# Kernel optimization log

Measured on AMD Instinct MI355X. Metric: run time of the kernel, lower is better.

## Reference

```python
import jax, jax.numpy as jnp
import numpy as np

D, NH, NL, NP, NLAYERS, DFF = 256, 8, 4, 4, 6, 1024
HD = D // NH
SHAPES = [(100, 100), (50, 50), (25, 25), (13, 13)]  # (H, W) per level
B = 4


def layernorm(x, w, b):
    m = x.mean(-1, keepdims=True)
    v = ((x - m) ** 2).mean(-1, keepdims=True)
    return (x - m) / jnp.sqrt(v + 1e-5) * w + b


def bilinear_sample(vl, loc, H, W):
    # vl: [B, H*W, NH, HD] level values; loc: [B, Lq, NH, NP, 2] normalized in [0,1]
    # matches F.grid_sample(bilinear, zeros padding, align_corners=False)
    bsz, Lq = loc.shape[0], loc.shape[1]
    px = loc[..., 0] * W - 0.5
    py = loc[..., 1] * H - 0.5
    x0 = jnp.floor(px); y0 = jnp.floor(py)
    wx1 = px - x0; wy1 = py - y0
    out = jnp.zeros((bsz, Lq, NH, NP, HD), vl.dtype)
    for xi, wx in ((x0, 1.0 - wx1), (x0 + 1.0, wx1)):
        for yi, wy in ((y0, 1.0 - wy1), (y0 + 1.0, wy1)):
            valid = (xi >= 0) & (xi < W) & (yi >= 0) & (yi < H)
            xc = jnp.clip(xi, 0, W - 1).astype(jnp.int32)
            yc = jnp.clip(yi, 0, H - 1).astype(jnp.int32)
            idx = yc * W + xc                                   # [B,Lq,NH,NP]
            idx2 = idx.transpose(0, 1, 3, 2).reshape(bsz, Lq * NP, NH, 1)
            g = jnp.take_along_axis(vl, idx2, axis=1)           # [B,Lq*NP,NH,HD]
            g = g.reshape(bsz, Lq, NP, NH, HD).transpose(0, 1, 3, 2, 4)
            w = (wx * wy * valid.astype(vl.dtype))[..., None]
            out = out + g * w
    return out


def get_reference_points(bsz):
    refs = []
    for (H, W) in SHAPES:
        ry = (jnp.arange(H, dtype=jnp.float32) + 0.5) / H
        rx = (jnp.arange(W, dtype=jnp.float32) + 0.5) / W
        gy, gx = jnp.meshgrid(ry, rx, indexing='ij')
        refs.append(jnp.stack([gx.reshape(-1), gy.reshape(-1)], -1))
    ref = jnp.concatenate(refs, 0)                              # [Len, 2]
    return jnp.broadcast_to(ref[None, :, None, :], (bsz, ref.shape[0], NL, 2))


def ms_deform_attn(query, src, ref, starts, so_w, so_b, aw_w, aw_b, vp_w, vp_b, op_w, op_b):
    bsz, Lq, _ = query.shape
    value = (src @ vp_w + vp_b).reshape(bsz, -1, NH, HD)
    offsets = (query @ so_w + so_b).reshape(bsz, Lq, NH, NL, NP, 2)
    aw = (query @ aw_w + aw_b).reshape(bsz, Lq, NH, NL * NP)
    aw = jax.nn.softmax(aw, -1).reshape(bsz, Lq, NH, NL, NP)
    normalizer = jnp.array([[W, H] for (H, W) in SHAPES], jnp.float32)  # x by W, y by H
    loc = ref[:, :, None, :, None, :] + offsets / normalizer[None, None, None, :, None, :]
    out = jnp.zeros((bsz, Lq, NH, HD), query.dtype)
    for l, (H, W) in enumerate(SHAPES):
        vl = value[:, starts[l]:starts[l] + H * W]
        sampled = bilinear_sample(vl, loc[:, :, :, l], H, W)    # [B,Lq,NH,NP,HD]
        out = out + jnp.einsum('blhp,blhpd->blhd', aw[:, :, :, l], sampled)
    return out.reshape(bsz, Lq, D) @ op_w + op_b


def setup_inputs():
    key = jax.random.key(0)
    ks = iter(jax.random.split(key, 64))
    d = {}
    for i, (H, W) in enumerate(SHAPES):
        d[f'src{i}'] = jax.random.normal(next(ks), (B, D, H, W), jnp.float32)
        d[f'pos{i}'] = jax.random.normal(next(ks), (B, D, H, W), jnp.float32)
    d['level_embed'] = jax.random.normal(next(ks), (NL, D), jnp.float32)
    d['so_w'] = jax.random.normal(next(ks), (NLAYERS, D, NH * NL * NP * 2), jnp.float32) * 0.005
    d['so_b'] = jax.random.normal(next(ks), (NLAYERS, NH * NL * NP * 2), jnp.float32) * 0.1
    d['aw_w'] = jax.random.normal(next(ks), (NLAYERS, D, NH * NL * NP), jnp.float32) * 0.02
    d['aw_b'] = jnp.zeros((NLAYERS, NH * NL * NP), jnp.float32)
    d['vp_w'] = jax.random.normal(next(ks), (NLAYERS, D, D), jnp.float32) * 0.02
    d['vp_b'] = jnp.zeros((NLAYERS, D), jnp.float32)
    d['op_w'] = jax.random.normal(next(ks), (NLAYERS, D, D), jnp.float32) * 0.02
    d['op_b'] = jnp.zeros((NLAYERS, D), jnp.float32)
    d['n1_w'] = jnp.ones((NLAYERS, D), jnp.float32)
    d['n1_b'] = jnp.zeros((NLAYERS, D), jnp.float32)
    d['f1_w'] = jax.random.normal(next(ks), (NLAYERS, D, DFF), jnp.float32) * 0.02
    d['f1_b'] = jnp.zeros((NLAYERS, DFF), jnp.float32)
    d['f2_w'] = jax.random.normal(next(ks), (NLAYERS, DFF, D), jnp.float32) * 0.02
    d['f2_b'] = jnp.zeros((NLAYERS, D), jnp.float32)
    d['n2_w'] = jnp.ones((NLAYERS, D), jnp.float32)
    d['n2_b'] = jnp.zeros((NLAYERS, D), jnp.float32)
    return d


def reference(src0, src1, src2, src3, pos0, pos1, pos2, pos3, level_embed,
              so_w, so_b, aw_w, aw_b, vp_w, vp_b, op_w, op_b,
              n1_w, n1_b, f1_w, f1_b, f2_w, f2_b, n2_w, n2_b):
    srcs = [src0, src1, src2, src3]
    poss = [pos0, pos1, pos2, pos3]
    bsz = src0.shape[0]
    src_flat, pos_flat, starts, off = [], [], [], 0
    for l, ((H, W), s, p) in enumerate(zip(SHAPES, srcs, poss)):
        starts.append(off); off += H * W
        src_flat.append(s.reshape(bsz, D, H * W).transpose(0, 2, 1))
        pos_flat.append(p.reshape(bsz, D, H * W).transpose(0, 2, 1) + level_embed[l][None, None, :])
    src = jnp.concatenate(src_flat, 1)                          # [B, Len, D]
    pos = jnp.concatenate(pos_flat, 1)
    ref = get_reference_points(bsz)
    for i in range(NLAYERS):
        q = src + pos
        attn = ms_deform_attn(q, src, ref, starts,
                              so_w[i], so_b[i], aw_w[i], aw_b[i],
                              vp_w[i], vp_b[i], op_w[i], op_b[i])
        src = layernorm(src + attn, n1_w[i], n1_b[i])
        h = jax.nn.relu(src @ f1_w[i] + f1_b[i]) @ f2_w[i] + f2_b[i]
        src = layernorm(src + h, n2_w[i], n2_b[i])
    level_start_index = jnp.array(starts, jnp.int64 if jax.config.jax_enable_x64 else jnp.int32)
    return src, level_start_index
```

## Files before the change

### kernel.cpp

```cpp
#include <hip/hip_runtime.h>

#define D 256
#define L_TOT 13294

typedef __attribute__((ext_vector_type(8))) __bf16 bf16x8;
typedef __attribute__((ext_vector_type(4))) float f32x4;
typedef __attribute__((ext_vector_type(2))) float f32x2;

__device__ __forceinline__ float bf2f(unsigned short u) {
    return __uint_as_float(((unsigned int)u) << 16);
}
__device__ __forceinline__ unsigned short f2bf(float f) {
    unsigned int u = __float_as_uint(f);
    u += 0x7FFFu + ((u >> 16) & 1u);
    return (unsigned short)(u >> 16);
}
__device__ __forceinline__ f32x2 bfpair(unsigned int d) {
    f32x2 r;
    r.x = __uint_as_float(d << 16);
    r.y = __uint_as_float(d & 0xFFFF0000u);
    return r;
}
__device__ __forceinline__ f32x2 fma2(f32x2 a, float w, f32x2 c) {
    return __builtin_elementwise_fma(a, (f32x2){w, w}, c);
}

__global__ void probe_k(const unsigned short* __restrict__ u, int n, int* __restrict__ flag)
{
    __shared__ int cnt;
    if (threadIdx.x == 0) cnt = 0;
    __syncthreads();
    int c = 0;
    for (int i = threadIdx.x; i < n; i += 256) {
        const int e = (u[i] >> 7) & 0xFF;
        if (e == 0 || (e >= 96 && e <= 150)) ++c;
    }
    atomicAdd(&cnt, c);
    __syncthreads();
    if (threadIdx.x == 0) *flag = (cnt * 10 > n * 9) ? 1 : 0;
}

__global__ __launch_bounds__(256) void convert_k(
    const void* __restrict__ src, unsigned short* __restrict__ dst, int n,
    const int* __restrict__ flag)
{
    const int i = blockIdx.x * 256 + threadIdx.x;
    if (i >= n) return;
    if (*flag) dst[i] = ((const unsigned short*)src)[i];
    else       dst[i] = f2bf(((const float*)src)[i]);
}

__global__ __launch_bounds__(256) void convt_k(
    const void* __restrict__ src, unsigned short* __restrict__ dst,
    int K, int N, int L, const int* __restrict__ flag)
{
    const long e = (long)blockIdx.x * 256 + threadIdx.x;
    const long tot = (long)L * K * N;
    if (e >= tot) return;
    const int per = K * N;
    const int li = (int)(e / per);
    const int r  = (int)(e - (long)li * per);
    const int n  = r / K;
    const int k  = r - n * K;
    const long s = (long)li * per + (long)k * N + n;
    dst[e] = (*flag) ? ((const unsigned short*)src)[s]
                     : f2bf(((const float*)src)[s]);
}

__global__ __launch_bounds__(256) void flatten_k(
    const void* __restrict__ s0, const void* __restrict__ s1,
    const void* __restrict__ s2, const void* __restrict__ s3,
    const int* __restrict__ flag, unsigned short* __restrict__ state)
{
    const long e = (long)blockIdx.x * 256 + threadIdx.x;
    const int d = (int)(e & 255);
    const long tok = e >> 8;
    const int b = (int)(tok / L_TOT);
    const int t = (int)(tok - (long)b * L_TOT);
    const void *sp;
    int hw, idx;
    if (t < 10000)      { sp = s0; hw = 10000; idx = t;          }
    else if (t < 12500) { sp = s1; hw = 2500;  idx = t - 10000;  }
    else if (t < 13125) { sp = s2; hw = 625;   idx = t - 12500;  }
    else                { sp = s3; hw = 169;   idx = t - 13125;  }
    const long a = ((long)b * D + d) * hw + idx;
    state[e] = (*flag) ? ((const unsigned short*)sp)[a]
                       : f2bf(((const float*)sp)[a]);
}

__global__ __launch_bounds__(256) void posconst_k(
    const void* __restrict__ p0, const void* __restrict__ p1,
    const void* __restrict__ p2, const void* __restrict__ p3,
    const unsigned short* __restrict__ lev, const int* __restrict__ flag,
    unsigned short* __restrict__ posc)
{
    const long e = (long)blockIdx.x * 256 + threadIdx.x;
    const int d = (int)(e & 255);
    const long tok = e >> 8;
    const int b = (int)(tok / L_TOT);
    const int t = (int)(tok - (long)b * L_TOT);
    const void *pp;
    int hw, idx, l;
    if (t < 10000)      { pp = p0; hw = 10000; idx = t;          l = 0; }
    else if (t < 12500) { pp = p1; hw = 2500;  idx = t - 10000;  l = 1; }
    else if (t < 13125) { pp = p2; hw = 625;   idx = t - 12500;  l = 2; }
    else                { pp = p3; hw = 169;   idx = t - 13125;  l = 3; }
    const long a = ((long)b * D + d) * hw + idx;
    const float pv = (*flag) ? bf2f(((const unsigned short*)pp)[a])
                             : ((const float*)pp)[a];
    posc[e] = f2bf(pv + bf2f(lev[l * D + d]));
}

__global__ __launch_bounds__(256) void addq_k(
    const unsigned short* __restrict__ x, const unsigned short* __restrict__ p,
    unsigned short* __restrict__ q, long n8)
{
    const long e = (long)blockIdx.x * 256 + threadIdx.x;
    if (e >= n8) return;
    const uint4 xv = ((const uint4*)x)[e];
    const uint4 pv = ((const uint4*)p)[e];
    uint4 o;
#define ADDPK(a, b) ({ const f32x2 fa = bfpair(a), fb = bfpair(b); \
        (unsigned int)f2bf(fb.x + fa.x) | ((unsigned int)f2bf(fb.y + fa.y) << 16); })
    o.x = ADDPK(xv.x, pv.x); o.y = ADDPK(xv.y, pv.y);
    o.z = ADDPK(xv.z, pv.z); o.w = ADDPK(xv.w, pv.w);
#undef ADDPK
    ((uint4*)q)[e] = o;
}

__global__ __launch_bounds__(256) void posflat_k(
    const void* __restrict__ p0, const void* __restrict__ p1,
    const void* __restrict__ p2, const void* __restrict__ p3,
    const unsigned short* __restrict__ lev, const int* __restrict__ flag,
    const unsigned short* __restrict__ x, unsigned short* __restrict__ q)
{
    const long e = (long)blockIdx.x * 256 + threadIdx.x;
    const int d = (int)(e & 255);
    const long tok = e >> 8;
    const int b = (int)(tok / L_TOT);
    const int t = (int)(tok - (long)b * L_TOT);
    const void *pp;
    int hw, idx, l;
    if (t < 10000)      { pp = p0; hw = 10000; idx = t;          l = 0; }
    else if (t < 12500) { pp = p1; hw = 2500;  idx = t - 10000;  l = 1; }
    else if (t < 13125) { pp = p2; hw = 625;   idx = t - 12500;  l = 2; }
    else                { pp = p3; hw = 169;   idx = t - 13125;  l = 3; }
    const long a = ((long)b * D + d) * hw + idx;
    const float pv = (*flag) ? bf2f(((const unsigned short*)pp)[a])
                             : ((const float*)pp)[a];
    q[e] = f2bf(pv + bf2f(lev[l * D + d]) + bf2f(x[e]));
}

template<bool RELU, bool RESID>
__device__ __forceinline__ void gemm_core(
    const unsigned short* __restrict__ A, int ldA,
    const unsigned short* __restrict__ Bt, int ldB,
    const unsigned short* __restrict__ bias,
    const unsigned short* resid,
    unsigned short* out, int ldO,
    long M, int K, int col0, long row0,
    unsigned short* As, unsigned short* Bs)
{
    const int tid = threadIdx.x;
    const int l  = tid & 63;
    const int w  = tid >> 6;
    const int wm = w >> 1, wn = w & 1;

    f32x4 acc[4][4];
#pragma unroll
    for (int i = 0; i < 4; ++i)
#pragma unroll
        for (int j = 0; j < 4; ++j) acc[i][j] = (f32x4){0.f, 0.f, 0.f, 0.f};

    const int sr = tid >> 3;
    const int sg = tid & 7;

    for (int k0 = 0; k0 < K; k0 += 64) {
#pragma unroll
        for (int i = 0; i < 4; ++i) {
            const int r = i * 32 + sr;
            long arow = row0 + r; if (arow >= M) arow = M - 1;
            const int ke = k0 + ((sg ^ (r & 7)) << 3);
            const unsigned short* ga = A  + arow * (long)ldA + ke;
            const unsigned short* gb = Bt + (long)(col0 + r) * ldB + ke;
            __builtin_amdgcn_global_load_lds(
                (const __attribute__((address_space(1))) void*)ga,
                (__attribute__((address_space(3))) void*)(As + i * 2048 + w * 512),
                16, 0, 0);
            __builtin_amdgcn_global_load_lds(
                (const __attribute__((address_space(1))) void*)gb,
                (__attribute__((address_space(3))) void*)(Bs + i * 2048 + w * 512),
                16, 0, 0);
        }
        __syncthreads();
#pragma unroll
        for (int ks = 0; ks < 2; ++ks) {
            const int cc  = ks * 4 + (l >> 4);
            const int swz = ((cc ^ (l & 7)) << 4);
            bf16x8 af[4], bfr[4];
#pragma unroll
            for (int mi = 0; mi < 4; ++mi) {
                const int ar = wm * 64 + mi * 16 + (l & 15);
                af[mi] = *(const bf16x8*)((const char*)As + ar * 128 + swz);
            }
#pragma unroll
            for (int ni = 0; ni < 4; ++ni) {
                const int br = wn * 64 + ni * 16 + (l & 15);
                bfr[ni] = *(const bf16x8*)((const char*)Bs + br * 128 + swz);
            }
#pragma unroll
            for (int mi = 0; mi < 4; ++mi)
#pragma unroll
                for (int ni = 0; ni < 4; ++ni)
                    acc[mi][ni] = __builtin_amdgcn_mfma_f32_16x16x32_bf16(
                        bfr[ni], af[mi], acc[mi][ni], 0, 0, 0);
        }
        __syncthreads();
    }

#pragma unroll
    for (int mi = 0; mi < 4; ++mi) {
        const long rr = row0 + wm * 64 + mi * 16 + (l & 15);
        if (rr >= M) continue;
#pragma unroll
        for (int ni = 0; ni < 4; ++ni) {
            const int col = col0 + wn * 64 + ni * 16 + (l >> 4) * 4;
            f32x4 v = acc[mi][ni];
            if (bias) {
                const ushort4 b4 = *(const ushort4*)(bias + col);
                v[0] += bf2f(b4.x); v[1] += bf2f(b4.y);
                v[2] += bf2f(b4.z); v[3] += bf2f(b4.w);
            }
            if (RELU) {
                v[0] = fmaxf(v[0], 0.f); v[1] = fmaxf(v[1], 0.f);
                v[2] = fmaxf(v[2], 0.f); v[3] = fmaxf(v[3], 0.f);
            }
            if (RESID) {
                const ushort4 r4 = *(const ushort4*)(resid + rr * (long)ldO + col);
                v[0] += bf2f(r4.x); v[1] += bf2f(r4.y);
                v[2] += bf2f(r4.z); v[3] += bf2f(r4.w);
            }
            ushort4 o;
            o.x = f2bf(v[0]); o.y = f2bf(v[1]); o.z = f2bf(v[2]); o.w = f2bf(v[3]);
            *(ushort4*)(out + rr * (long)ldO + col) = o;
        }
    }
}

template<bool RELU, bool RESID>
__global__ __launch_bounds__(256, 3) void mgemm_k(
    const unsigned short* __restrict__ A, int ldA,
    const unsigned short* __restrict__ Bt, int ldB,
    const unsigned short* __restrict__ bias,
    const unsigned short* resid,
    unsigned short* out, int ldOut,
    long M, int K)
{
    __shared__ unsigned short As[8192];
    __shared__ unsigned short Bs[8192];
    gemm_core<RELU, RESID>(A, ldA, Bt, ldB, bias, resid, out, ldOut,
                           M, K, blockIdx.x * 128, (long)blockIdx.y * 128, As, Bs);
}

__global__ __launch_bounds__(256, 3) void mgemm3_k(
    const unsigned short* __restrict__ state, const unsigned short* __restrict__ q,
    const unsigned short* __restrict__ Wv,  const unsigned short* __restrict__ bv,
    const unsigned short* __restrict__ Wso, const unsigned short* __restrict__ bso,
    const unsigned short* __restrict__ Waw, const unsigned short* __restrict__ baw,
    unsigned short* valo, unsigned short* offo, unsigned short* awo, long M)
{
    __shared__ unsigned short As[8192];
    __shared__ unsigned short Bs[8192];
    const int cx = blockIdx.x * 128;
    const long row0 = (long)blockIdx.y * 128;
    if (cx < 256)
        gemm_core<false, false>(state, D, Wv, D, bv, nullptr, valo, D,
                                M, D, cx, row0, As, Bs);
    else if (cx < 512)
        gemm_core<false, false>(q, D, Wso, D, bso, nullptr, offo, D,
                                M, D, cx - 256, row0, As, Bs);
    else
        gemm_core<false, false>(q, D, Waw, D, baw, nullptr, awo, 128,
                                M, D, 0, row0, As, Bs);
}

template<bool QOUT>
__global__ __launch_bounds__(256, 3) void mgemmln_k(
    const unsigned short* __restrict__ A, int ldA,
    const unsigned short* __restrict__ Bt, int ldB,
    const unsigned short* __restrict__ bias,
    const unsigned short* resid,
    const unsigned short* __restrict__ gamma,
    const unsigned short* __restrict__ beta,
    unsigned short* outp,
    const unsigned short* __restrict__ posc,
    unsigned short* __restrict__ qout,
    long M, int K)
{
    __shared__ unsigned short As[64 * 64];
    __shared__ unsigned short Bs[256 * 64];
    __shared__ float red[2][4][4][16];
    const int tid = threadIdx.x;
    const int l = tid & 63;
    const int w = tid >> 6;
    const long row0 = (long)blockIdx.x * 64;

    f32x4 acc[4][4];
#pragma unroll
    for (int i = 0; i < 4; ++i)
#pragma unroll
        for (int j = 0; j < 4; ++j) acc[i][j] = (f32x4){0.f, 0.f, 0.f, 0.f};

    for (int k0 = 0; k0 < K; k0 += 64) {
#pragma unroll
        for (int i = 0; i < 10; ++i) {
            const int c = i * 256 + tid;
            const unsigned short* gsrc;
            unsigned short* ldst;
            if (i < 2) {
                const int r = c >> 3, grp = c & 7;
                long ar = row0 + r; if (ar >= M) ar = M - 1;
                gsrc = A + ar * (long)ldA + (k0 + ((grp ^ (r & 7)) << 3));
                ldst = As + (c << 3);
            } else {
                const int r = (c >> 3) - 64, grp = c & 7;
                gsrc = Bt + (long)r * ldB + (k0 + ((grp ^ (r & 7)) << 3));
                ldst = Bs + ((c - 512) << 3);
            }
            __builtin_amdgcn_global_load_lds(
                (const __attribute__((address_space(1))) void*)gsrc,
                (__attribute__((address_space(3))) void*)ldst, 16, 0, 0);
        }
        __syncthreads();
#pragma unroll
        for (int ks = 0; ks < 2; ++ks) {
            const int cc = ks * 4 + (l >> 4);
            bf16x8 af[4], bfr[4];
#pragma unroll
            for (int mi = 0; mi < 4; ++mi) {
                const int ar = mi * 16 + (l & 15);
                af[mi] = *(const bf16x8*)((const char*)As + ar * 128 + ((cc ^ (ar & 7)) << 4));
            }
#pragma unroll
            for (int ni = 0; ni < 4; ++ni) {
                const int br = w * 64 + ni * 16 + (l & 15);
                bfr[ni] = *(const bf16x8*)((const char*)Bs + br * 128 + ((cc ^ (br & 7)) << 4));
            }
#pragma unroll
            for (int mi = 0; mi < 4; ++mi)
#pragma unroll
                for (int ni = 0; ni < 4; ++ni)
                    acc[mi][ni] = __builtin_amdgcn_mfma_f32_16x16x32_bf16(
                        bfr[ni], af[mi], acc[mi][ni], 0, 0, 0);
        }
        __syncthreads();
    }

#pragma unroll
    for (int mi = 0; mi < 4; ++mi) {
        const long rr = row0 + mi * 16 + (l & 15);
        const long rrc = (rr < M) ? rr : (M - 1);
#pragma unroll
        for (int ni = 0; ni < 4; ++ni) {
            const int col = w * 64 + ni * 16 + (l >> 4) * 4;
            const ushort4 b4 = *(const ushort4*)(bias + col);
            const ushort4 r4 = *(const ushort4*)(resid + rrc * D + col);
            acc[mi][ni][0] = bf2f(f2bf(acc[mi][ni][0] + bf2f(b4.x) + bf2f(r4.x)));
            acc[mi][ni][1] = bf2f(f2bf(acc[mi][ni][1] + bf2f(b4.y) + bf2f(r4.y)));
            acc[mi][ni][2] = bf2f(f2bf(acc[mi][ni][2] + bf2f(b4.z) + bf2f(r4.z)));
            acc[mi][ni][3] = bf2f(f2bf(acc[mi][ni][3] + bf2f(b4.w) + bf2f(r4.w)));
        }
    }
#pragma unroll
    for (int mi = 0; mi < 4; ++mi) {
        float s = 0.f, qq = 0.f;
#pragma unroll
        for (int ni = 0; ni < 4; ++ni)
#pragma unroll
            for (int r = 0; r < 4; ++r) {
                const float v = acc[mi][ni][r];
                s += v; qq += v * v;
            }
        s += __shfl_xor(s, 16);  s += __shfl_xor(s, 32);
        qq += __shfl_xor(qq, 16); qq += __shfl_xor(qq, 32);
        if (l < 16) { red[0][w][mi][l] = s; red[1][w][mi][l] = qq; }
    }
    __syncthreads();
    float mean[4], rstd[4];
#pragma unroll
    for (int mi = 0; mi < 4; ++mi) {
        const int r16 = l & 15;
        const float s = red[0][0][mi][r16] + red[0][1][mi][r16]
                      + red[0][2][mi][r16] + red[0][3][mi][r16];
        const float qq = red[1][0][mi][r16] + red[1][1][mi][r16]
                       + red[1][2][mi][r16] + red[1][3][mi][r16];
        const float mn = s * (1.f / D);
        const float var = qq * (1.f / D) - mn * mn;
        mean[mi] = mn;
        rstd[mi] = rsqrtf(var + 1e-5f);
    }
#pragma unroll
    for (int mi = 0; mi < 4; ++mi) {
        const long rr = row0 + mi * 16 + (l & 15);
        if (rr >= M) continue;
#pragma unroll
        for (int ni = 0; ni < 4; ++ni) {
            const int col = w * 64 + ni * 16 + (l >> 4) * 4;
            const ushort4 g4 = *(const ushort4*)(gamma + col);
            const ushort4 e4 = *(const ushort4*)(beta + col);
            ushort4 o;
            o.x = f2bf((acc[mi][ni][0] - mean[mi]) * rstd[mi] * bf2f(g4.x) + bf2f(e4.x));
            o.y = f2bf((acc[mi][ni][1] - mean[mi]) * rstd[mi] * bf2f(g4.y) + bf2f(e4.y));
            o.z = f2bf((acc[mi][ni][2] - mean[mi]) * rstd[mi] * bf2f(g4.z) + bf2f(e4.z));
            o.w = f2bf((acc[mi][ni][3] - mean[mi]) * rstd[mi] * bf2f(g4.w) + bf2f(e4.w));
            *(ushort4*)(outp + rr * D + col) = o;
            if (QOUT) {
                const ushort4 p4 = *(const ushort4*)(posc + rr * D + col);
                ushort4 qo;
                qo.x = f2bf(bf2f(o.x) + bf2f(p4.x));
                qo.y = f2bf(bf2f(o.y) + bf2f(p4.y));
                qo.z = f2bf(bf2f(o.z) + bf2f(p4.z));
                qo.w = f2bf(bf2f(o.w) + bf2f(p4.w));
                *(ushort4*)(qout + rr * D + col) = qo;
            }
        }
    }
}

__global__ __launch_bounds__(256) void sample_k(
    const unsigned short* __restrict__ off, const unsigned short* __restrict__ aw,
    const unsigned short* __restrict__ val, unsigned short* __restrict__ attn)
{
    __shared__ __align__(16) int   cidx[128][4];
    __shared__ __align__(16) float cw[128][4];
    __shared__ float red[3][4][64];
    const long tok = blockIdx.x;
    const int tid = threadIdx.x;
    const int b = (int)(tok / L_TOT);
    const int t = (int)(tok - (long)b * L_TOT);

    if (tid < 128) {
        const int u = tid;
        const int lp = u & 15;
        const int mu = lp * 8 + (u >> 4);
        const int cswz = lp & 3;
        const float logit = bf2f(aw[tok * 128 + u]);
        float m = logit;
#pragma unroll
        for (int mk = 1; mk < 16; mk <<= 1) m = fmaxf(m, __shfl_xor(m, mk));
        const float e = expf(logit - m);
        float s = e;
#pragma unroll
        for (int mk = 1; mk < 16; mk <<= 1) s += __shfl_xor(s, mk);
        const float a = e / s;
        int st0, W0;
        if (t < 10000)      { st0 = 0;     W0 = 100; }
        else if (t < 12500) { st0 = 10000; W0 = 50;  }
        else if (t < 13125) { st0 = 12500; W0 = 25;  }
        else                { st0 = 13125; W0 = 13;  }
        const int i0 = t - st0;
        const int yy = i0 / W0;
        const int xx = i0 - yy * W0;
        const float gx = (xx + 0.5f) / (float)W0;
        const float gy = (yy + 0.5f) / (float)W0;
        const int lv = (u >> 2) & 3;
        const int Wv  = (lv == 0) ? 100 : (lv == 1) ? 50 : (lv == 2) ? 25 : 13;
        const int stl = (lv == 0) ? 0 : (lv == 1) ? 10000 : (lv == 2) ? 12500 : 13125;
        const unsigned int op = *(const unsigned int*)(off + tok * 256 + 2 * u);
        const float ox = bf2f((unsigned short)op);
        const float oy = bf2f((unsigned short)(op >> 16));
        const float px = (gx + ox / (float)Wv) * Wv - 0.5f;
        const float py = (gy + oy / (float)Wv) * Wv - 0.5f;
        const float fx = floorf(px), fy = floorf(py);
        const float wx1 = px - fx, wy1 = py - fy;
        const int x0 = (int)fx, y0 = (int)fy;
#pragma unroll
        for (int c = 0; c < 4; ++c) {
            const int xi = x0 + (c & 1);
            const int yi = y0 + (c >> 1);
            const float wgt = ((c & 1) ? wx1 : 1.f - wx1) * ((c >> 1) ? wy1 : 1.f - wy1);
            const bool ok = (xi >= 0) && (xi < Wv) && (yi >= 0) && (yi < Wv);
            cidx[mu][c ^ cswz] = ok ? ((stl + yi * Wv + xi) << 9) : 0;
            cw[mu][c ^ cswz]   = ok ? wgt * a : 0.f;
        }
    }
    __syncthreads();
    const int g = tid >> 6;
    const int l = tid & 63;
    const int h = l >> 3;
    const int q = l & 7;
    const char* vb = (const char*)val + ((long)b * L_TOT) * 512 + h * 64 + q * 8;
    f32x2 A01 = {0.f, 0.f}, A23 = {0.f, 0.f};
#pragma unroll
    for (int j = 0; j < 4; ++j) {
        const int mu = (j * 4 + g) * 8 + h;
        const int4   ci = *(const int4*)(&cidx[mu][0]);
        const float4 wv = *(const float4*)(&cw[mu][0]);
        const uint2 d0 = *(const uint2*)(vb + ci.x);
        const uint2 d1 = *(const uint2*)(vb + ci.y);
        const uint2 d2 = *(const uint2*)(vb + ci.z);
        const uint2 d3 = *(const uint2*)(vb + ci.w);
        A01 = fma2(bfpair(d0.x), wv.x, A01);  A23 = fma2(bfpair(d0.y), wv.x, A23);
        A01 = fma2(bfpair(d1.x), wv.y, A01);  A23 = fma2(bfpair(d1.y), wv.y, A23);
        A01 = fma2(bfpair(d2.x), wv.z, A01);  A23 = fma2(bfpair(d2.y), wv.z, A23);
        A01 = fma2(bfpair(d3.x), wv.w, A01);  A23 = fma2(bfpair(d3.y), wv.w, A23);
    }
    if (g) {
        red[g - 1][0][l] = A01.x; red[g - 1][1][l] = A01.y;
        red[g - 1][2][l] = A23.x; red[g - 1][3][l] = A23.y;
    }
    __syncthreads();
    if (g == 0) {
        float a0 = A01.x, a1 = A01.y, a2 = A23.x, a3 = A23.y;
#pragma unroll
        for (int p = 0; p < 3; ++p) {
            a0 += red[p][0][l]; a1 += red[p][1][l];
            a2 += red[p][2][l]; a3 += red[p][3][l];
        }
        ushort4 o;
        o.x = f2bf(a0); o.y = f2bf(a1); o.z = f2bf(a2); o.w = f2bf(a3);
        *(ushort4*)(attn + tok * 256 + h * 32 + q * 4) = o;
    }
}

template<bool QOUT>
__global__ __launch_bounds__(256) void ln_k(
    const unsigned short* __restrict__ y,
    const unsigned short* __restrict__ g, const unsigned short* __restrict__ bb,
    unsigned short* __restrict__ out,
    const unsigned short* __restrict__ posc, unsigned short* __restrict__ qout,
    long nt)
{
    const int wv = threadIdx.x >> 6;
    const int lane = threadIdx.x & 63;
    const long tok = (long)blockIdx.x * 4 + wv;
    if (tok >= nt) return;
    const ushort4 v4 = *(const ushort4*)(y + tok * D + lane * 4);
    const float v0 = bf2f(v4.x), v1 = bf2f(v4.y), v2 = bf2f(v4.z), v3 = bf2f(v4.w);
    float s = v0 + v1 + v2 + v3;
#pragma unroll
    for (int m = 1; m < 64; m <<= 1) s += __shfl_xor(s, m);
    const float mean = s * (1.f / D);
    const float d0 = v0 - mean, d1 = v1 - mean, d2 = v2 - mean, d3 = v3 - mean;
    float q = d0 * d0 + d1 * d1 + d2 * d2 + d3 * d3;
#pragma unroll
    for (int m = 1; m < 64; m <<= 1) q += __shfl_xor(q, m);
    const float rstd = rsqrtf(q * (1.f / D) + 1e-5f);
    const int c0 = lane * 4;
    ushort4 o;
    o.x = f2bf(d0 * rstd * bf2f(g[c0 + 0]) + bf2f(bb[c0 + 0]));
    o.y = f2bf(d1 * rstd * bf2f(g[c0 + 1]) + bf2f(bb[c0 + 1]));
    o.z = f2bf(d2 * rstd * bf2f(g[c0 + 2]) + bf2f(bb[c0 + 2]));
    o.w = f2bf(d3 * rstd * bf2f(g[c0 + 3]) + bf2f(bb[c0 + 3]));
    *(ushort4*)(out + tok * D + c0) = o;
    if (QOUT) {
        const ushort4 p4 = *(const ushort4*)(posc + tok * D + c0);
        ushort4 qo;
        qo.x = f2bf(bf2f(o.x) + bf2f(p4.x));
        qo.y = f2bf(bf2f(o.y) + bf2f(p4.y));
        qo.z = f2bf(bf2f(o.z) + bf2f(p4.z));
        qo.w = f2bf(bf2f(o.w) + bf2f(p4.w));
        *(ushort4*)(qout + tok * D + c0) = qo;
    }
}

__global__ __launch_bounds__(256) void finalize_k(
    const unsigned short* __restrict__ state, float* __restrict__ out, long osz)
{
    const long e = (long)blockIdx.x * 256 + threadIdx.x;
    const long n0 = osz - 4;
    if (e < n0) out[e] = bf2f(state[e]);
    if (e < 4) {
        const float st[4] = {0.f, 10000.f, 12500.f, 13125.f};
        out[n0 + e] = st[e];
    }
}

extern "C" void kernel_launch(void* const* d_in, const int* in_sizes, int n_in,
                              void* d_out, int out_size, void* d_ws, size_t ws_size,
                              hipStream_t stream)
{
    (void)n_in;
    const long osz = (long)out_size;
    const long nt = (osz - 4) / D;
    const int nlayers = in_sizes[9] / (D * D);
    const int dff = in_sizes[19] / (nlayers * D);

    char* ws = (char*)d_ws;
    int* flag = (int*)ws;  ws += 256;
    unsigned short* wc = (unsigned short*)ws;
    long off[25]; long acc_off = 0;
    for (int i = 8; i <= 24; ++i) { off[i] = acc_off; acc_off += in_sizes[i]; }
    ws += ((acc_off * 2 + 255) / 256) * 256;
    const size_t SZ_BF = (size_t)nt * D * 2;
    unsigned short* state     = (unsigned short*)ws;  ws += SZ_BF;
    unsigned short* val_b     = (unsigned short*)ws;  ws += SZ_BF;
    unsigned short* offy_b    = (unsigned short*)ws;  ws += SZ_BF;
    unsigned short* posattn_b = (unsigned short*)ws;  ws += SZ_BF;
    unsigned short* aw_b      = (unsigned short*)ws;  ws += (size_t)nt * 128 * 2;
    unsigned short* hbuf = val_b;

    const size_t used_base = (size_t)((char*)aw_b - (char*)d_ws) + (size_t)nt * 128 * 2;
    const bool have_posc  = (ws_size >= used_base + SZ_BF);
    const bool have_hfull = (ws_size >= used_base + SZ_BF + 4 * SZ_BF);
    unsigned short* posc  = (unsigned short*)((char*)d_ws + used_base);
    unsigned short* hfull = (unsigned short*)((char*)d_ws + used_base + SZ_BF);

    probe_k<<<1, 256, 0, stream>>>((const unsigned short*)d_in[8], in_sizes[8], flag);

    const int vecIdx[11] = {8, 10, 12, 14, 16, 17, 18, 20, 22, 23, 24};
    for (int j = 0; j < 11; ++j) {
        const int i = vecIdx[j];
        convert_k<<<(in_sizes[i] + 255) / 256, 256, 0, stream>>>(
            d_in[i], wc + off[i], in_sizes[i], flag);
    }
    const int matIdx[6] = {9, 11, 13, 15, 19, 21};
    const int matK[6]   = {D, D, D, D, D, dff};
    const int matN[6]   = {D, 128, D, D, dff, D};
    for (int j = 0; j < 6; ++j) {
        const int i = matIdx[j];
        convt_k<<<(in_sizes[i] + 255) / 256, 256, 0, stream>>>(
            d_in[i], wc + off[i], matK[j], matN[j], nlayers, flag);
    }

    flatten_k<<<(int)nt, 256, 0, stream>>>(
        d_in[0], d_in[2], d_in[4], d_in[6], flag, state);
    if (have_posc)
        posconst_k<<<(int)nt, 256, 0, stream>>>(
            d_in[1], d_in[3], d_in[5], d_in[7], wc + off[8], flag, posc);

    const int MB = (int)((nt + 127) / 128);
    const int FB = (int)((nt + 63) / 64);
    const int LB = (int)((nt + 3) / 4);
    const long n8 = (long)nt * D / 8;
    const int AB = (int)((n8 + 255) / 256);
    const int dh = dff / 2;

    if (have_posc)
        addq_k<<<AB, 256, 0, stream>>>(state, posc, posattn_b, n8);

    for (int i = 0; i < nlayers; ++i) {
        if (!have_posc)
            posflat_k<<<(int)nt, 256, 0, stream>>>(
                d_in[1], d_in[3], d_in[5], d_in[7], wc + off[8], flag, state, posattn_b);
        mgemm3_k<<<dim3(5, MB), 256, 0, stream>>>(
            state, posattn_b,
            wc + off[13] + (long)i * D * D,   wc + off[14] + i * D,
            wc + off[9]  + (long)i * D * 256, wc + off[10] + i * 256,
            wc + off[11] + (long)i * D * 128, wc + off[12] + i * 128,
            val_b, offy_b, aw_b, nt);
        sample_k<<<(int)nt, 256, 0, stream>>>(offy_b, aw_b, val_b, posattn_b);
        if (have_hfull) {
            mgemmln_k<false><<<FB, 256, 0, stream>>>(
                posattn_b, D, wc + off[15] + (long)i * D * D, D, wc + off[16] + i * D,
                state, wc + off[17] + i * D, wc + off[18] + i * D, state,
                nullptr, nullptr, nt, D);
            mgemm_k<true, false><<<dim3(dff / 128, MB), 256, 0, stream>>>(
                state, D, wc + off[19] + (long)i * D * dff, D, wc + off[20] + i * dff,
                nullptr, hfull, dff, nt, D);
            if (have_posc && i + 1 < nlayers)
                mgemmln_k<true><<<FB, 256, 0, stream>>>(
                    hfull, dff, wc + off[21] + (long)i * dff * D, dff,
                    wc + off[22] + i * D, state,
                    wc + off[23] + i * D, wc + off[24] + i * D, state,
                    posc, posattn_b, nt, dff);
            else
                mgemmln_k<false><<<FB, 256, 0, stream>>>(
                    hfull, dff, wc + off[21] + (long)i * dff * D, dff,
                    wc + off[22] + i * D, state,
                    wc + off[23] + i * D, wc + off[24] + i * D, state,
                    nullptr, nullptr, nt, dff);
        } else {
            mgemm_k<false, true><<<dim3(2, MB), 256, 0, stream>>>(
                posattn_b, D, wc + off[15] + (long)i * D * D, D, wc + off[16] + i * D,
                state, offy_b, D, nt, D);
            ln_k<false><<<LB, 256, 0, stream>>>(offy_b, wc + off[17] + i * D,
                wc + off[18] + i * D, state, nullptr, nullptr, nt);
            mgemm_k<true, false><<<dim3(dh / 128, MB), 256, 0, stream>>>(
                state, D, wc + off[19] + (long)i * D * dff, D, wc + off[20] + i * dff,
                nullptr, hbuf, dh, nt, D);
            mgemm_k<false, true><<<dim3(2, MB), 256, 0, stream>>>(
                hbuf, dh, wc + off[21] + (long)i * dff * D, dff, wc + off[22] + i * D,
                state, posattn_b, D, nt, dh);
            mgemm_k<true, false><<<dim3(dh / 128, MB), 256, 0, stream>>>(
                state, D, wc + off[19] + (long)i * D * dff + (long)dh * D, D,
                wc + off[20] + i * dff + dh, nullptr, hbuf, dh, nt, D);
            mgemm_k<false, true><<<dim3(2, MB), 256, 0, stream>>>(
                hbuf, dh, wc + off[21] + (long)i * dff * D + dh, dff, nullptr,
                posattn_b, posattn_b, D, nt, dh);
            if (have_posc && i + 1 < nlayers)
                ln_k<true><<<LB, 256, 0, stream>>>(posattn_b, wc + off[23] + i * D,
                    wc + off[24] + i * D, state, posc, posattn_b, nt);
            else
                ln_k<false><<<LB, 256, 0, stream>>>(posattn_b, wc + off[23] + i * D,
                    wc + off[24] + i * D, state, nullptr, nullptr, nt);
        }
    }

    finalize_k<<<(int)((osz - 4 + 255) / 256), 256, 0, stream>>>(
        state, (float*)d_out, osz);
}
```

Baseline: 2.406 ms.

## Process two tokens per sampling block with 16-byte gathers and shuffle reduction

The deformable-attention sampling kernel now handles two query tokens per 256-thread block instead of one. Every thread of the block computes sampling coordinates and weights. The gather phase uses 16-byte value loads (8 bf16 channels) per corner instead of 8-byte loads, and half the point-slot partial sums are combined with a cross-lane shuffle before a smaller shared-memory reduction. This halves the block count, doubles per-thread load width and cuts LDS reduction traffic. The trade-off is more registers per thread and fewer independent gathers in flight per channel.

After: 2.150 ms. 1.12x faster.

```diff
diff --git a/kernel.cpp b/kernel.cpp
--- a/kernel.cpp
+++ b/kernel.cpp
@@ -429,18 +429,21 @@
 
 __global__ __launch_bounds__(256) void sample_k(
     const unsigned short* __restrict__ off, const unsigned short* __restrict__ aw,
-    const unsigned short* __restrict__ val, unsigned short* __restrict__ attn)
-{
-    __shared__ __align__(16) int   cidx[128][4];
-    __shared__ __align__(16) float cw[128][4];
-    __shared__ float red[3][4][64];
-    const long tok = blockIdx.x;
+    const unsigned short* __restrict__ val, unsigned short* __restrict__ attn,
+    long nt)
+{
+    __shared__ __align__(16) int   cidx[2][128][4];
+    __shared__ __align__(16) float cw[2][128][4];
+    __shared__ __align__(16) float red[2][32][8];
     const int tid = threadIdx.x;
-    const int b = (int)(tok / L_TOT);
-    const int t = (int)(tok - (long)b * L_TOT);
-
-    if (tid < 128) {
-        const int u = tid;
+
+    {
+        const int tk = tid >> 7;
+        const int u  = tid & 127;
+        long tok = (long)blockIdx.x * 2 + tk;
+        if (tok >= nt) tok = nt - 1;
+        const int b = (int)(tok / L_TOT);
+        const int t = (int)(tok - (long)b * L_TOT);
         const int lp = u & 15;
         const int mu = lp * 8 + (u >> 4);
         const int cswz = lp & 3;
@@ -480,46 +483,68 @@
             const int yi = y0 + (c >> 1);
             const float wgt = ((c & 1) ? wx1 : 1.f - wx1) * ((c >> 1) ? wy1 : 1.f - wy1);
             const bool ok = (xi >= 0) && (xi < Wv) && (yi >= 0) && (yi < Wv);
-            cidx[mu][c ^ cswz] = ok ? ((stl + yi * Wv + xi) << 9) : 0;
-            cw[mu][c ^ cswz]   = ok ? wgt * a : 0.f;
+            cidx[tk][mu][c ^ cswz] = ok ? ((stl + yi * Wv + xi) << 9) : 0;
+            cw[tk][mu][c ^ cswz]   = ok ? wgt * a : 0.f;
         }
     }
     __syncthreads();
-    const int g = tid >> 6;
-    const int l = tid & 63;
-    const int h = l >> 3;
-    const int q = l & 7;
-    const char* vb = (const char*)val + ((long)b * L_TOT) * 512 + h * 64 + q * 8;
-    f32x2 A01 = {0.f, 0.f}, A23 = {0.f, 0.f};
+
+    const int tk = tid >> 7;
+    long tok = (long)blockIdx.x * 2 + tk;
+    if (tok >= nt) tok = nt - 1;
+    const int b = (int)(tok / L_TOT);
+    const int r = tid & 127;
+    const int slot = r >> 5;
+    const int l32 = r & 31;
+    const int h  = l32 >> 2;
+    const int q4 = l32 & 3;
+    const char* valc = (const char*)val;
+    const unsigned int vbase = (unsigned int)b * (unsigned int)(L_TOT * 512)
+                             + (unsigned int)(h * 64 + q4 * 16);
+    f32x2 ac[4];
+#pragma unroll
+    for (int k = 0; k < 4; ++k) ac[k] = (f32x2){0.f, 0.f};
 #pragma unroll
     for (int j = 0; j < 4; ++j) {
-        const int mu = (j * 4 + g) * 8 + h;
-        const int4   ci = *(const int4*)(&cidx[mu][0]);
-        const float4 wv = *(const float4*)(&cw[mu][0]);
-        const uint2 d0 = *(const uint2*)(vb + ci.x);
-        const uint2 d1 = *(const uint2*)(vb + ci.y);
-        const uint2 d2 = *(const uint2*)(vb + ci.z);
-        const uint2 d3 = *(const uint2*)(vb + ci.w);
-        A01 = fma2(bfpair(d0.x), wv.x, A01);  A23 = fma2(bfpair(d0.y), wv.x, A23);
-        A01 = fma2(bfpair(d1.x), wv.y, A01);  A23 = fma2(bfpair(d1.y), wv.y, A23);
-        A01 = fma2(bfpair(d2.x), wv.z, A01);  A23 = fma2(bfpair(d2.y), wv.z, A23);
-        A01 = fma2(bfpair(d3.x), wv.w, A01);  A23 = fma2(bfpair(d3.y), wv.w, A23);
-    }
-    if (g) {
-        red[g - 1][0][l] = A01.x; red[g - 1][1][l] = A01.y;
-        red[g - 1][2][l] = A23.x; red[g - 1][3][l] = A23.y;
+        const int mu = (j * 4 + slot) * 8 + h;
+        const int4   ci = *(const int4*)(&cidx[tk][mu][0]);
+        const float4 wv = *(const float4*)(&cw[tk][mu][0]);
+        const uint4 d0 = *(const uint4*)(valc + (vbase + (unsigned int)ci.x));
+        const uint4 d1 = *(const uint4*)(valc + (vbase + (unsigned int)ci.y));
+        const uint4 d2 = *(const uint4*)(valc + (vbase + (unsigned int)ci.z));
+        const uint4 d3 = *(const uint4*)(valc + (vbase + (unsigned int)ci.w));
+        ac[0] = fma2(bfpair(d0.x), wv.x, ac[0]); ac[1] = fma2(bfpair(d0.y), wv.x, ac[1]);
+        ac[2] = fma2(bfpair(d0.z), wv.x, ac[2]); ac[3] = fma2(bfpair(d0.w), wv.x, ac[3]);
+        ac[0] = fma2(bfpair(d1.x), wv.y, ac[0]); ac[1] = fma2(bfpair(d1.y), wv.y, ac[1]);
+        ac[2] = fma2(bfpair(d1.z), wv.y, ac[2]); ac[3] = fma2(bfpair(d1.w), wv.y, ac[3]);
+        ac[0] = fma2(bfpair(d2.x), wv.z, ac[0]); ac[1] = fma2(bfpair(d2.y), wv.z, ac[1]);
+        ac[2] = fma2(bfpair(d2.z), wv.z, ac[2]); ac[3] = fma2(bfpair(d2.w), wv.z, ac[3]);
+        ac[0] = fma2(bfpair(d3.x), wv.w, ac[0]); ac[1] = fma2(bfpair(d3.y), wv.w, ac[1]);
+        ac[2] = fma2(bfpair(d3.z), wv.w, ac[2]); ac[3] = fma2(bfpair(d3.w), wv.w, ac[3]);
+    }
+#pragma unroll
+    for (int k = 0; k < 4; ++k) {
+        ac[k].x += __shfl_xor(ac[k].x, 32);
+        ac[k].y += __shfl_xor(ac[k].y, 32);
+    }
+    if (r >= 64 && r < 96) {
+#pragma unroll
+        for (int k = 0; k < 4; ++k) {
+            red[tk][l32][2 * k]     = ac[k].x;
+            red[tk][l32][2 * k + 1] = ac[k].y;
+        }
     }
     __syncthreads();
-    if (g == 0) {
-        float a0 = A01.x, a1 = A01.y, a2 = A23.x, a3 = A23.y;
-#pragma unroll
-        for (int p = 0; p < 3; ++p) {
-            a0 += red[p][0][l]; a1 += red[p][1][l];
-            a2 += red[p][2][l]; a3 += red[p][3][l];
-        }
-        ushort4 o;
-        o.x = f2bf(a0); o.y = f2bf(a1); o.z = f2bf(a2); o.w = f2bf(a3);
-        *(ushort4*)(attn + tok * 256 + h * 32 + q * 4) = o;
+    if (r < 32) {
+        uint4 o;
+        unsigned int* op = &o.x;
+#pragma unroll
+        for (int k = 0; k < 4; ++k) {
+            const float v0 = ac[k].x + red[tk][l32][2 * k];
+            const float v1 = ac[k].y + red[tk][l32][2 * k + 1];
+            op[k] = (unsigned int)f2bf(v0) | ((unsigned int)f2bf(v1) << 16);
+        }
+        *(uint4*)(attn + tok * 256 + h * 32 + q4 * 8) = o;
     }
 }
 
@@ -631,6 +656,7 @@
 
     const int MB = (int)((nt + 127) / 128);
     const int FB = (int)((nt + 63) / 64);
+    const int SB = (int)((nt + 1) / 2);
     const int LB = (int)((nt + 3) / 4);
     const long n8 = (long)nt * D / 8;
     const int AB = (int)((n8 + 255) / 256);
@@ -649,7 +675,7 @@
             wc + off[9]  + (long)i * D * 256, wc + off[10] + i * 256,
             wc + off[11] + (long)i * D * 128, wc + off[12] + i * 128,
             val_b, offy_b, aw_b, nt);
-        sample_k<<<(int)nt, 256, 0, stream>>>(offy_b, aw_b, val_b, posattn_b);
+        sample_k<<<SB, 256, 0, stream>>>(offy_b, aw_b, val_b, posattn_b, nt);
         if (have_hfull) {
             mgemmln_k<false><<<FB, 256, 0, stream>>>(
                 posattn_b, D, wc + off[15] + (long)i * D * D, D, wc + off[16] + i * D,
```
